# Kernel tuning notes

Measured on AMD Instinct MI355X. Metric: run time of the kernel, lower is better.

The kernel has to match this reference:

```python
import jax, jax.numpy as jnp
import numpy as np
from jax import lax

E = 8      # embed dim
H = 8      # num heads (head_dim = 1)
EPS = 1e-5


def pe_row(pos, d=E):
    # PositionalEncoding quirk: original adds pe[:, x.size(1), :] -> a SINGLE row at index L.
    i = jnp.arange(0, d, 2, dtype=jnp.float32)
    div = jnp.exp(i * (-np.log(10000.0) / d))
    row = jnp.zeros((d,), jnp.float32)
    row = row.at[0::2].set(jnp.sin(pos * div))
    row = row.at[1::2].set(jnp.cos(pos * div))
    return row


def layernorm(x, g, b):
    mu = jnp.mean(x, axis=-1, keepdims=True)
    var = jnp.mean((x - mu) ** 2, axis=-1, keepdims=True)
    return (x - mu) / jnp.sqrt(var + EPS) * g + b


def mha(q, k, v, wi, bi, wo, bo):
    # torch nn.MultiheadAttention, batch_first, eval mode (dropout off)
    d = E // H
    qp = q @ wi[:E].T + bi[:E]
    kp = k @ wi[E:2 * E].T + bi[E:2 * E]
    vp = v @ wi[2 * E:].T + bi[2 * E:]
    sh = lambda x: x.reshape(x.shape[0], x.shape[1], H, d).transpose(0, 2, 1, 3)
    qh, kh, vh = sh(qp), sh(kp), sh(vp)
    scores = jnp.einsum('bhqd,bhkd->bhqk', qh, kh) / np.sqrt(d)
    attn = jax.nn.softmax(scores, axis=-1)
    o = jnp.einsum('bhqk,bhkd->bhqd', attn, vh)
    B, _, L, _ = o.shape
    o = o.transpose(0, 2, 1, 3).reshape(B, L, E)
    return o @ wo.T + bo


def conv1d_k1p1(x, w, b):
    # Conv1d kernel_size=1, padding=1 (conv_tgt branch), then permute to (B, L, C)
    y = lax.conv_general_dilated(x, w, (1,), [(1, 1)],
                                 dimension_numbers=('NCW', 'OIW', 'NCW'))
    return (y + b[None, :, None]).transpose(0, 2, 1)


def setup_inputs() -> dict:
    key = jax.random.key(0)
    ks = jax.random.split(key, 32)
    B = 8192
    r = lambda i, shape, s=0.05: jax.random.normal(ks[i], shape, jnp.float32) * s
    return {
        'eeg': jax.random.normal(ks[0], (B, 2, 20, 118), jnp.float32),
        'pupil': jax.random.normal(ks[1], (B, 2, 30), jnp.float32),
        'speech': jax.random.normal(ks[2], (B, 2, 30), jnp.float32),
        'action': jax.random.normal(ks[3], (B, 2, 30), jnp.float32),
        'location': jax.random.normal(ks[4], (B, 3, 30), jnp.float32),
        'tgt': jax.random.normal(ks[5], (B, 30), jnp.float32),
        'eeg_conv_w': r(6, (E, 2, 20, 2), 0.1), 'eeg_conv_b': r(7, (E,)),
        'psa_conv_w': r(8, (E, 2, 1), 0.3), 'psa_conv_b': r(9, (E,)),
        'loc_conv_w': r(10, (E, 3, 1), 0.3), 'loc_conv_b': r(11, (E,)),
        'tgt_conv_w': r(12, (E, 1, 1), 0.3), 'tgt_conv_b': r(13, (E,)),
        'norm_g': jnp.ones((E,), jnp.float32), 'norm_b': jnp.zeros((E,), jnp.float32),
        'cross_in_w': r(14, (3 * E, E), 0.3), 'cross_in_b': r(15, (3 * E,)),
        'cross_out_w': r(16, (E, E), 0.3), 'cross_out_b': r(17, (E,)),
        'self_in_w': r(18, (3 * E, E), 0.3), 'self_in_b': r(19, (3 * E,)),
        'self_out_w': r(20, (E, E), 0.3), 'self_out_b': r(21, (E,)),
        'out_in_w': r(22, (3 * E, E), 0.3), 'out_in_b': r(23, (3 * E,)),
        'out_out_w': r(24, (E, E), 0.3), 'out_out_b': r(25, (E,)),
        'fc1_w': r(26, (90, 256), 0.1), 'fc1_b': r(27, (90,)),
    }


def reference(eeg, pupil, speech, action, location, tgt,
              eeg_conv_w, eeg_conv_b, psa_conv_w, psa_conv_b,
              loc_conv_w, loc_conv_b, tgt_conv_w, tgt_conv_b,
              norm_g, norm_b,
              cross_in_w, cross_in_b, cross_out_w, cross_out_b,
              self_in_w, self_in_b, self_out_w, self_out_b,
              out_in_w, out_in_b, out_out_w, out_out_b,
              fc1_w, fc1_b):
    B = eeg.shape[0]
    # eeg conv2d: (B,2,20,118) -> (B,8,1,30) -> (B,30,8)
    e = lax.conv_general_dilated(eeg, eeg_conv_w, (1, 4), 'VALID',
                                 dimension_numbers=('NCHW', 'OIHW', 'NCHW'))
    e = (e + eeg_conv_b[None, :, None, None]).squeeze(2).transpose(0, 2, 1)
    # pupil/speech/action/location (raw len 30 -> conv_tgt branch -> seq 32)
    p = conv1d_k1p1(pupil, psa_conv_w, psa_conv_b)
    s = conv1d_k1p1(speech, psa_conv_w, psa_conv_b)
    a = conv1d_k1p1(action, psa_conv_w, psa_conv_b)
    l = conv1d_k1p1(location, loc_conv_w, loc_conv_b)
    # positional encoding adds single row pe[L]
    e = e + pe_row(30.0)
    p = p + pe_row(32.0)
    s = s + pe_row(32.0)
    a = a + pe_row(32.0)
    l = l + pe_row(32.0)

    cross = lambda q, kv: mha(q, kv, kv, cross_in_w, cross_in_b, cross_out_w, cross_out_b)
    selfa = lambda x: mha(x, x, x, self_in_w, self_in_b, self_out_w, self_out_b)
    nrm = lambda x: layernorm(x, norm_g, norm_b)

    eeg_final = (nrm(cross(e, p)) + nrm(cross(e, a)) + nrm(cross(e, l))
                 + nrm(selfa(e)) + nrm(cross(e, s)))
    pupil_final = (nrm(cross(p, e)) + nrm(cross(p, a)) + nrm(cross(p, l))
                   + nrm(selfa(p)) + nrm(cross(p, s)))
    s_cross_l = nrm(cross(s, l))
    speech_final = (nrm(cross(s, e)) + nrm(cross(s, p)) + nrm(cross(s, a))
                    + s_cross_l)  # original omits speech_self
    # original bug: action_cross_location = norm(speech_cross_location)
    action_final = (nrm(cross(a, e)) + nrm(cross(a, p)) + s_cross_l
                    + nrm(selfa(a)) + nrm(cross(a, s)))
    concatenated = jnp.concatenate([eeg_final, pupil_final, action_final, speech_final], axis=1)  # (B,126,8)

    t = conv1d_k1p1(tgt[:, None, :], tgt_conv_w, tgt_conv_b)  # (B,32,8)
    t = t + pe_row(32.0)
    out = mha(t, concatenated, concatenated, out_in_w, out_in_b, out_out_w, out_out_b)  # (B,32,8)
    out = out.reshape(B, 32 * E) @ fc1_w.T + fc1_b  # (B,90)
    out = out.reshape(B, 30, 3).transpose(0, 2, 1)  # (B,3,30)
    return jax.nn.softmax(out, axis=1)
```

## Files before the change

### kernel.cpp

```cpp
#include <hip/hip_runtime.h>
#include <cstdint>
#include <cstddef>

#define NT 256
#define LOG2E 1.4426950408889634f

typedef float v2f __attribute__((ext_vector_type(2)));
typedef float v4f __attribute__((ext_vector_type(4)));

#if defined(__has_builtin)
#  if __has_builtin(__builtin_amdgcn_exp2f)
#    define EXP2F(x) __builtin_amdgcn_exp2f(x)
#  else
#    define EXP2F(x) exp2f(x)
#  endif
#else
#  define EXP2F(x) exp2f(x)
#endif

enum {
  OFF_EEGB = 0,
  OFF_PSAW = 8,
  OFF_PSAB = 24,
  OFF_LOCW = 32,
  OFF_LOCB = 56,
  OFF_TGTW = 64,
  OFF_TGTB = 72,
  OFF_NG   = 80,
  OFF_NB   = 88,
  OFF_CINW = 96,
  OFF_CINB = 288,
  OFF_COUTW= 312,
  OFF_COUTB= 376,
  OFF_SINW = 384,
  OFF_SINB = 576,
  OFF_SOUTW= 600,
  OFF_SOUTB= 664,
  OFF_OINW = 672,
  OFF_OINB = 864,
  OFF_OOUTW= 888,
  OFF_OOUTB= 952,
  OFF_FC1B = 960,
  OFF_PE30 = 1052,
  OFF_PE32 = 1060,
  OFF_Ebuf = 1068,
  OFF_Pbuf = 1308,
  OFF_Sbuf = 1564,
  OFF_Abuf = 1820,
  OFF_Lbuf = 2076,
  OFF_Tbuf = 2332,
  OFF_CAT  = 2588,
  OFF_QP   = 3596,
  OFF_KS   = 3852,
  OFF_VS   = 4396,
  OFF_FCO  = 4940,
  SM_TOTAL = 5032,
  OFF_EEGW = OFF_KS,
};

struct MhaDesc { int Lq, Lk, kstart, qoff, kvoff, wset, dst1, dst2, flags; };

#define EB 0
#define PB 30
#define AB 62
#define SB 94
static __device__ const MhaDesc g_desc[20] = {
  {30, 32, 0, OFF_Ebuf, OFF_Pbuf, 0, EB, -1, 3},
  {30, 32, 0, OFF_Ebuf, OFF_Abuf, 0, EB, -1, 3},
  {30, 32, 0, OFF_Ebuf, OFF_Lbuf, 0, EB, -1, 3},
  {30, 30, 0, OFF_Ebuf, OFF_Ebuf, 1, EB, -1, 3},
  {30, 32, 0, OFF_Ebuf, OFF_Sbuf, 0, EB, -1, 3},
  {32, 30, 0, OFF_Pbuf, OFF_Ebuf, 0, PB, -1, 3},
  {32, 32, 0, OFF_Pbuf, OFF_Abuf, 0, PB, -1, 3},
  {32, 32, 0, OFF_Pbuf, OFF_Lbuf, 0, PB, -1, 3},
  {32, 32, 0, OFF_Pbuf, OFF_Pbuf, 1, PB, -1, 3},
  {32, 32, 0, OFF_Pbuf, OFF_Sbuf, 0, PB, -1, 3},
  {32, 30, 0, OFF_Sbuf, OFF_Ebuf, 0, SB, -1, 3},
  {32, 32, 0, OFF_Sbuf, OFF_Pbuf, 0, SB, -1, 3},
  {32, 32, 0, OFF_Sbuf, OFF_Abuf, 0, SB, -1, 3},
  {32, 32, 0, OFF_Sbuf, OFF_Lbuf, 0, SB, AB, 3},
  {32, 30, 0, OFF_Abuf, OFF_Ebuf, 0, AB, -1, 3},
  {32, 32, 0, OFF_Abuf, OFF_Pbuf, 0, AB, -1, 3},
  {32, 32, 0, OFF_Abuf, OFF_Abuf, 1, AB, -1, 3},
  {32, 32, 0, OFF_Abuf, OFF_Sbuf, 0, AB, -1, 3},
  {32, 64, 0,  OFF_Tbuf, OFF_CAT, 2, -1, -1, 1},
  {32, 62, 64, OFF_Tbuf, OFF_CAT, 2, -1, -1, 2},
};

__device__ __forceinline__ float grp8_sum(float v) {
  v += __shfl_xor(v, 1);
  v += __shfl_xor(v, 2);
  v += __shfl_xor(v, 4);
  return v;
}

__device__ __forceinline__ float dot8(const float* __restrict__ x,
                                      const float* __restrict__ w, float bias) {
  v4f xa = *(const v4f*)x, xb = *(const v4f*)(x + 4);
  v4f wa = *(const v4f*)w, wb = *(const v4f*)(w + 4);
  v4f p = xa * wa;
  p += xb * wb;
  v2f q = p.xy + p.zw;
  return bias + q.x + q.y;
}

template<int LK>
__device__ __forceinline__ void attn_accum(float qq, const float* __restrict__ Kp,
                                           const float* __restrict__ Vp,
                                           v4f& l4, v4f& A4) {
  constexpr int N4 = LK >> 2;
  #pragma unroll
  for (int k4 = 0; k4 < N4; k4++) {
    v4f kk = *(const v4f*)(Kp + 4 * k4);
    v4f vv = *(const v4f*)(Vp + 4 * k4);
    v4f sc = kk * qq;
    v4f ee = { EXP2F(sc.x), EXP2F(sc.y), EXP2F(sc.z), EXP2F(sc.w) };
    l4 += ee;
    A4 += ee * vv;
  }
  if constexpr ((LK & 3) != 0) {
    v2f kk = *(const v2f*)(Kp + 4 * N4);
    v2f vv = *(const v2f*)(Vp + 4 * N4);
    v2f sc = kk * qq;
    v2f ee = { EXP2F(sc.x), EXP2F(sc.y) };
    l4.xy = l4.xy + ee;
    A4.xy = A4.xy + ee * vv;
  }
}

__global__ __launch_bounds__(NT, 8) void cmt_kernel(
    const float* __restrict__ eeg, const float* __restrict__ pupil,
    const float* __restrict__ speech, const float* __restrict__ action,
    const float* __restrict__ location, const float* __restrict__ tgt,
    const float* __restrict__ eeg_w, const float* __restrict__ eeg_b,
    const float* __restrict__ psa_w, const float* __restrict__ psa_b,
    const float* __restrict__ loc_w, const float* __restrict__ loc_b,
    const float* __restrict__ tgt_w, const float* __restrict__ tgt_b,
    const float* __restrict__ ng, const float* __restrict__ nb,
    const float* __restrict__ cin_w, const float* __restrict__ cin_b,
    const float* __restrict__ cout_w, const float* __restrict__ cout_b,
    const float* __restrict__ sin_w, const float* __restrict__ sin_b,
    const float* __restrict__ sout_w, const float* __restrict__ sout_b,
    const float* __restrict__ oin_w, const float* __restrict__ oin_b,
    const float* __restrict__ oout_w, const float* __restrict__ oout_b,
    const float* __restrict__ fc1_w, const float* __restrict__ fc1_b,
    float* __restrict__ out)
{
  __shared__ __align__(16) float sm[SM_TOTAL];
  const int tid = threadIdx.x;
  const int b = blockIdx.x;

#define CP(off, p, n) for (int i = tid; i < (n); i += NT) sm[(off)+i] = (p)[i]
#define CPQ(off, p, n, nq) for (int i = tid; i < (n); i += NT) sm[(off)+i] = (p)[i] * ((i < (nq)) ? LOG2E : 1.0f)

  for (int i = tid; i < 640; i += NT) sm[OFF_EEGW + i] = eeg_w[(i & 7) * 80 + (i >> 3)];
  CP(OFF_EEGB, eeg_b, 8);
  CP(OFF_PSAW, psa_w, 16);   CP(OFF_PSAB, psa_b, 8);
  CP(OFF_LOCW, loc_w, 24);   CP(OFF_LOCB, loc_b, 8);
  CP(OFF_TGTW, tgt_w, 8);    CP(OFF_TGTB, tgt_b, 8);
  CP(OFF_NG, ng, 8);         CP(OFF_NB, nb, 8);
  CPQ(OFF_CINW, cin_w, 192, 64);  CPQ(OFF_CINB, cin_b, 24, 8);
  CP(OFF_COUTW, cout_w, 64); CP(OFF_COUTB, cout_b, 8);
  CPQ(OFF_SINW, sin_w, 192, 64);  CPQ(OFF_SINB, sin_b, 24, 8);
  CP(OFF_SOUTW, sout_w, 64); CP(OFF_SOUTB, sout_b, 8);
  CPQ(OFF_OINW, oin_w, 192, 64);  CPQ(OFF_OINB, oin_b, 24, 8);
  CP(OFF_OOUTW, oout_w, 64); CP(OFF_OOUTB, oout_b, 8);
  CP(OFF_FC1B, fc1_b, 90);
  for (int i = tid; i < 1008; i += NT) sm[OFF_CAT + i] = 0.f;
  if (tid < 16) {
    const float divs[4] = {1.f, 0.1f, 0.01f, 0.001f};
    float pos = (tid < 8) ? 30.f : 32.f;
    int e = tid & 7;
    float x = pos * divs[e >> 1];
    float v = (e & 1) ? cosf(x) : sinf(x);
    sm[((tid < 8) ? OFF_PE30 : OFF_PE32) + e] = v;
  }
  __syncthreads();

  if (tid < 240) {
    int w = tid >> 3, o = tid & 7;
    const float* ep = eeg + (size_t)b * 4720 + 4 * w;
    const float* wt = sm + OFF_EEGW + o;
    float acc = sm[OFF_EEGB + o];
    #pragma unroll
    for (int i = 0; i < 2; i++)
      #pragma unroll
      for (int kh = 0; kh < 20; kh++) {
        float2 x = *(const float2*)(ep + i * 2360 + kh * 118);
        int ik = i * 20 + kh;
        acc = fmaf(x.x, wt[ik * 16], fmaf(x.y, wt[ik * 16 + 8], acc));
      }
    sm[OFF_Ebuf + w * 8 + o] = acc + sm[OFF_PE30 + o];
  }
  {
    int t = tid >> 3, o = tid & 7;
    bool inb = (t >= 1 && t <= 30);
    int ti = t - 1;
    float pe = sm[OFF_PE32 + o];
    float w0 = sm[OFF_PSAW + 2 * o], w1 = sm[OFF_PSAW + 2 * o + 1];
    float pb = sm[OFF_PSAB + o];
    float vp = pb, vs = pb, va = pb;
    float vl = sm[OFF_LOCB + o], vt = sm[OFF_TGTB + o];
    if (inb) {
      const float* pp = pupil    + (size_t)b * 60 + ti;
      const float* sp = speech   + (size_t)b * 60 + ti;
      const float* ap = action   + (size_t)b * 60 + ti;
      const float* lp = location + (size_t)b * 90 + ti;
      vp = fmaf(pp[0], w0, fmaf(pp[30], w1, vp));
      vs = fmaf(sp[0], w0, fmaf(sp[30], w1, vs));
      va = fmaf(ap[0], w0, fmaf(ap[30], w1, va));
      vl = fmaf(lp[0],  sm[OFF_LOCW + 3 * o],     vl);
      vl = fmaf(lp[30], sm[OFF_LOCW + 3 * o + 1], vl);
      vl = fmaf(lp[60], sm[OFF_LOCW + 3 * o + 2], vl);
      vt = fmaf(tgt[(size_t)b * 30 + ti], sm[OFF_TGTW + o], vt);
    }
    sm[OFF_Pbuf + tid] = vp + pe;
    sm[OFF_Sbuf + tid] = vs + pe;
    sm[OFF_Abuf + tid] = va + pe;
    sm[OFF_Lbuf + tid] = vl + pe;
    sm[OFF_Tbuf + tid] = vt + pe;
  }
  __syncthreads();

  float q_reg = 0.f;
  v4f l4 = {0.f, 0.f, 0.f, 0.f}, A4 = {0.f, 0.f, 0.f, 0.f};
  for (int mi = 0; mi < 20; mi++) {
    const MhaDesc d = g_desc[mi];
    int winO, binO, woutO, boutO;
    if (d.wset == 0)      { winO = OFF_CINW; binO = OFF_CINB; woutO = OFF_COUTW; boutO = OFF_COUTB; }
    else if (d.wset == 1) { winO = OFF_SINW; binO = OFF_SINB; woutO = OFF_SOUTW; boutO = OFF_SOUTB; }
    else                  { winO = OFF_OINW; binO = OFF_OINB; woutO = OFF_OOUTW; boutO = OFF_OOUTB; }

    if ((d.flags & 1) && tid < d.Lq * 8) {
      int r = tid >> 3, h = tid & 7;
      q_reg = dot8(sm + d.qoff + r * 8, sm + winO + h * 8, sm[binO + h]);
    }
    for (int idx = tid; idx < d.Lk * 8; idx += NT) {
      int r = idx >> 3, h = idx & 7;
      const float* x = sm + d.kvoff + (d.kstart + r) * 8;
      v4f xa = *(const v4f*)x, xb = *(const v4f*)(x + 4);
      const float* wk = sm + winO + 64 + h * 8;
      const float* wv = sm + winO + 128 + h * 8;
      v4f pk = xa * *(const v4f*)wk;  pk += xb * *(const v4f*)(wk + 4);
      v4f pv = xa * *(const v4f*)wv;  pv += xb * *(const v4f*)(wv + 4);
      v2f hk = pk.xy + pk.zw, hv = pv.xy + pv.zw;
      sm[OFF_KS + h * 68 + r] = sm[binO + 8 + h]  + hk.x + hk.y;
      sm[OFF_VS + h * 68 + r] = sm[binO + 16 + h] + hv.x + hv.y;
    }
    __syncthreads();

    if (tid < d.Lq * 8) {
      int e = tid & 7;
      if (d.flags & 1) { l4 = (v4f){0.f,0.f,0.f,0.f}; A4 = (v4f){0.f,0.f,0.f,0.f}; }
      const float* Kp = sm + OFF_KS + e * 68;
      const float* Vp = sm + OFF_VS + e * 68;
      switch (d.Lk) {
        case 32: attn_accum<32>(q_reg, Kp, Vp, l4, A4); break;
        case 30: attn_accum<30>(q_reg, Kp, Vp, l4, A4); break;
        case 64: attn_accum<64>(q_reg, Kp, Vp, l4, A4); break;
        case 62: attn_accum<62>(q_reg, Kp, Vp, l4, A4); break;
        default: __builtin_unreachable();
      }
      if (d.flags & 2) {
        v2f lp = l4.xy + l4.zw, ap = A4.xy + A4.zw;
        float ov = (ap.x + ap.y) * __builtin_amdgcn_rcpf(lp.x + lp.y);
        sm[OFF_QP + tid] = ov;
        int gb = tid & ~7;
        float a = dot8(sm + OFF_QP + gb, sm + woutO + e * 8, sm[boutO + e]);
        if (d.dst1 >= 0) {
          int qi = tid >> 3;
          float mu = grp8_sum(a) * 0.125f;
          float dd = a - mu;
          float var = grp8_sum(dd * dd) * 0.125f;
          float nv = fmaf(dd * rsqrtf(var + 1e-5f), sm[OFF_NG + e], sm[OFF_NB + e]);
          sm[OFF_CAT + (d.dst1 + qi) * 8 + e] += nv;
          if (d.dst2 >= 0) sm[OFF_CAT + (d.dst2 + qi) * 8 + e] += nv;
        } else {
          sm[OFF_QP + tid] = a;
        }
      }
    }
    __syncthreads();
  }

  if (tid < 180) {
    int j = tid >> 1, p = tid & 1;
    const v4f* w4 = (const v4f*)(fc1_w + j * 256);
    const v4f* o4 = (const v4f*)(sm + OFF_QP);
    v4f acc4 = {0.f, 0.f, 0.f, 0.f};
    #pragma unroll 8
    for (int c = p; c < 64; c += 2) acc4 += o4[c] * w4[c];
    v2f a2 = acc4.xy + acc4.zw;
    float acc = a2.x + a2.y;
    acc += __shfl_xor(acc, 1);
    if (p == 0) sm[OFF_FCO + j] = acc + sm[OFF_FC1B + j];
  }
  __syncthreads();
  if (tid < 30) {
    float x0 = sm[OFF_FCO + 3 * tid], x1 = sm[OFF_FCO + 3 * tid + 1], x2 = sm[OFF_FCO + 3 * tid + 2];
    float m = fmaxf(x0, fmaxf(x1, x2));
    float e0 = __expf(x0 - m), e1 = __expf(x1 - m), e2 = __expf(x2 - m);
    float inv = __builtin_amdgcn_rcpf(e0 + e1 + e2);
    float* op = out + (size_t)b * 90;
    op[tid]      = e0 * inv;
    op[30 + tid] = e1 * inv;
    op[60 + tid] = e2 * inv;
  }
#undef CP
#undef CPQ
}

extern "C" void kernel_launch(void* const* d_in, const int* in_sizes, int n_in,
                              void* d_out, int out_size, void* d_ws, size_t ws_size,
                              hipStream_t stream) {
  (void)n_in; (void)out_size; (void)d_ws; (void)ws_size;
  int B = in_sizes[0] / 4720;
  cmt_kernel<<<B, NT, 0, stream>>>(
      (const float*)d_in[0],  (const float*)d_in[1],  (const float*)d_in[2],
      (const float*)d_in[3],  (const float*)d_in[4],  (const float*)d_in[5],
      (const float*)d_in[6],  (const float*)d_in[7],  (const float*)d_in[8],
      (const float*)d_in[9],  (const float*)d_in[10], (const float*)d_in[11],
      (const float*)d_in[12], (const float*)d_in[13], (const float*)d_in[14],
      (const float*)d_in[15], (const float*)d_in[16], (const float*)d_in[17],
      (const float*)d_in[18], (const float*)d_in[19], (const float*)d_in[20],
      (const float*)d_in[21], (const float*)d_in[22], (const float*)d_in[23],
      (const float*)d_in[24], (const float*)d_in[25], (const float*)d_in[26],
      (const float*)d_in[27], (const float*)d_in[28], (const float*)d_in[29],
      (float*)d_out);
}
```

Before: 304.3 us.

## Process two queries per thread and accumulate attention outputs in registers

```diff
diff --git a/kernel.cpp b/kernel.cpp
--- a/kernel.cpp
+++ b/kernel.cpp
@@ -51,40 +51,40 @@
   OFF_Tbuf = 2332,
   OFF_CAT  = 2588,
   OFF_QP   = 3596,
-  OFF_KS   = 3852,
-  OFF_VS   = 4396,
-  OFF_FCO  = 4940,
-  SM_TOTAL = 5032,
+  OFF_KS   = 3916,
+  OFF_VS   = 4460,
+  OFF_FCO  = 5004,
+  SM_TOTAL = 5096,
   OFF_EEGW = OFF_KS,
 };
 
-struct MhaDesc { int Lq, Lk, kstart, qoff, kvoff, wset, dst1, dst2, flags; };
+struct MhaDesc { short Lq2, Lk, kstart, qoff, kvoff, wset, dst, flags; };
 
 #define EB 0
 #define PB 30
 #define AB 62
 #define SB 94
 static __device__ const MhaDesc g_desc[20] = {
-  {30, 32, 0, OFF_Ebuf, OFF_Pbuf, 0, EB, -1, 3},
-  {30, 32, 0, OFF_Ebuf, OFF_Abuf, 0, EB, -1, 3},
-  {30, 32, 0, OFF_Ebuf, OFF_Lbuf, 0, EB, -1, 3},
-  {30, 30, 0, OFF_Ebuf, OFF_Ebuf, 1, EB, -1, 3},
-  {30, 32, 0, OFF_Ebuf, OFF_Sbuf, 0, EB, -1, 3},
-  {32, 30, 0, OFF_Pbuf, OFF_Ebuf, 0, PB, -1, 3},
-  {32, 32, 0, OFF_Pbuf, OFF_Abuf, 0, PB, -1, 3},
-  {32, 32, 0, OFF_Pbuf, OFF_Lbuf, 0, PB, -1, 3},
-  {32, 32, 0, OFF_Pbuf, OFF_Pbuf, 1, PB, -1, 3},
-  {32, 32, 0, OFF_Pbuf, OFF_Sbuf, 0, PB, -1, 3},
-  {32, 30, 0, OFF_Sbuf, OFF_Ebuf, 0, SB, -1, 3},
-  {32, 32, 0, OFF_Sbuf, OFF_Pbuf, 0, SB, -1, 3},
-  {32, 32, 0, OFF_Sbuf, OFF_Abuf, 0, SB, -1, 3},
-  {32, 32, 0, OFF_Sbuf, OFF_Lbuf, 0, SB, AB, 3},
-  {32, 30, 0, OFF_Abuf, OFF_Ebuf, 0, AB, -1, 3},
-  {32, 32, 0, OFF_Abuf, OFF_Pbuf, 0, AB, -1, 3},
-  {32, 32, 0, OFF_Abuf, OFF_Abuf, 1, AB, -1, 3},
-  {32, 32, 0, OFF_Abuf, OFF_Sbuf, 0, AB, -1, 3},
-  {32, 64, 0,  OFF_Tbuf, OFF_CAT, 2, -1, -1, 1},
-  {32, 62, 64, OFF_Tbuf, OFF_CAT, 2, -1, -1, 2},
+  {15, 32, 0, OFF_Ebuf, OFF_Pbuf, 0, EB, 1|2|32},
+  {15, 32, 0, OFF_Ebuf, OFF_Abuf, 0, EB, 1|2},
+  {15, 32, 0, OFF_Ebuf, OFF_Lbuf, 0, EB, 1|2},
+  {15, 30, 0, OFF_Ebuf, OFF_Ebuf, 1, EB, 1|2},
+  {15, 32, 0, OFF_Ebuf, OFF_Sbuf, 0, EB, 1|2|4},
+  {16, 30, 0, OFF_Pbuf, OFF_Ebuf, 0, PB, 1|2|32},
+  {16, 32, 0, OFF_Pbuf, OFF_Abuf, 0, PB, 1|2},
+  {16, 32, 0, OFF_Pbuf, OFF_Lbuf, 0, PB, 1|2},
+  {16, 32, 0, OFF_Pbuf, OFF_Pbuf, 1, PB, 1|2},
+  {16, 32, 0, OFF_Pbuf, OFF_Sbuf, 0, PB, 1|2|4},
+  {16, 30, 0, OFF_Sbuf, OFF_Ebuf, 0, SB, 1|2|32},
+  {16, 32, 0, OFF_Sbuf, OFF_Pbuf, 0, SB, 1|2},
+  {16, 32, 0, OFF_Sbuf, OFF_Abuf, 0, SB, 1|2},
+  {16, 32, 0, OFF_Sbuf, OFF_Lbuf, 0, SB, 1|2|4|8},
+  {16, 30, 0, OFF_Abuf, OFF_Ebuf, 0, AB, 1|2|32},
+  {16, 32, 0, OFF_Abuf, OFF_Pbuf, 0, AB, 1|2},
+  {16, 32, 0, OFF_Abuf, OFF_Abuf, 1, AB, 1|2},
+  {16, 32, 0, OFF_Abuf, OFF_Sbuf, 0, AB, 1|2|4|16},
+  {16, 64, 0,  OFF_Tbuf, OFF_CAT, 2, -1, 1},
+  {16, 62, 64, OFF_Tbuf, OFF_CAT, 2, -1, 2},
 };
 
 __device__ __forceinline__ float grp8_sum(float v) {
@@ -97,34 +97,35 @@
 __device__ __forceinline__ float dot8(const float* __restrict__ x,
                                       const float* __restrict__ w, float bias) {
   v4f xa = *(const v4f*)x, xb = *(const v4f*)(x + 4);
-  v4f wa = *(const v4f*)w, wb = *(const v4f*)(w + 4);
-  v4f p = xa * wa;
-  p += xb * wb;
+  v4f p = xa * *(const v4f*)w;
+  p += xb * *(const v4f*)(w + 4);
   v2f q = p.xy + p.zw;
   return bias + q.x + q.y;
 }
 
 template<int LK>
-__device__ __forceinline__ void attn_accum(float qq, const float* __restrict__ Kp,
-                                           const float* __restrict__ Vp,
-                                           v4f& l4, v4f& A4) {
-  constexpr int N4 = LK >> 2;
+__device__ __forceinline__ void attn2(float q1, float q2,
+                                      const float* __restrict__ Kp,
+                                      const float* __restrict__ Vp,
+                                      v4f& la, v4f& Aa, v4f& lb, v4f& Ab) {
   #pragma unroll
-  for (int k4 = 0; k4 < N4; k4++) {
-    v4f kk = *(const v4f*)(Kp + 4 * k4);
-    v4f vv = *(const v4f*)(Vp + 4 * k4);
-    v4f sc = kk * qq;
-    v4f ee = { EXP2F(sc.x), EXP2F(sc.y), EXP2F(sc.z), EXP2F(sc.w) };
-    l4 += ee;
-    A4 += ee * vv;
+  for (int t = 0; t < (LK >> 2); t++) {
+    v4f kk = *(const v4f*)(Kp + 4 * t);
+    v4f vv = *(const v4f*)(Vp + 4 * t);
+    v4f s1 = kk * q1, s2 = kk * q2;
+    v4f e1 = { EXP2F(s1.x), EXP2F(s1.y), EXP2F(s1.z), EXP2F(s1.w) };
+    v4f e2 = { EXP2F(s2.x), EXP2F(s2.y), EXP2F(s2.z), EXP2F(s2.w) };
+    la += e1; Aa += e1 * vv;
+    lb += e2; Ab += e2 * vv;
   }
   if constexpr ((LK & 3) != 0) {
-    v2f kk = *(const v2f*)(Kp + 4 * N4);
-    v2f vv = *(const v2f*)(Vp + 4 * N4);
-    v2f sc = kk * qq;
-    v2f ee = { EXP2F(sc.x), EXP2F(sc.y) };
-    l4.xy = l4.xy + ee;
-    A4.xy = A4.xy + ee * vv;
+    v2f kk = *(const v2f*)(Kp + (LK & ~3));
+    v2f vv = *(const v2f*)(Vp + (LK & ~3));
+    v2f s1 = kk * q1, s2 = kk * q2;
+    v2f e1 = { EXP2F(s1.x), EXP2F(s1.y) };
+    v2f e2 = { EXP2F(s2.x), EXP2F(s2.y) };
+    la.xy = la.xy + e1; Aa.xy = Aa.xy + e1 * vv;
+    lb.xy = lb.xy + e2; Ab.xy = Ab.xy + e2 * vv;
   }
 }
 
@@ -153,7 +154,7 @@
 #define CP(off, p, n) for (int i = tid; i < (n); i += NT) sm[(off)+i] = (p)[i]
 #define CPQ(off, p, n, nq) for (int i = tid; i < (n); i += NT) sm[(off)+i] = (p)[i] * ((i < (nq)) ? LOG2E : 1.0f)
 
-  for (int i = tid; i < 640; i += NT) sm[OFF_EEGW + i] = eeg_w[(i & 7) * 80 + (i >> 3)];
+  for (int i = tid; i < 640; i += NT) sm[OFF_EEGW + (i / 80) * 84 + (i % 80)] = eeg_w[i];
   CP(OFF_EEGB, eeg_b, 8);
   CP(OFF_PSAW, psa_w, 16);   CP(OFF_PSAB, psa_b, 8);
   CP(OFF_LOCW, loc_w, 24);   CP(OFF_LOCB, loc_b, 8);
@@ -166,7 +167,6 @@
   CPQ(OFF_OINW, oin_w, 192, 64);  CPQ(OFF_OINB, oin_b, 24, 8);
   CP(OFF_OOUTW, oout_w, 64); CP(OFF_OOUTB, oout_b, 8);
   CP(OFF_FC1B, fc1_b, 90);
-  for (int i = tid; i < 1008; i += NT) sm[OFF_CAT + i] = 0.f;
   if (tid < 16) {
     const float divs[4] = {1.f, 0.1f, 0.01f, 0.001f};
     float pos = (tid < 8) ? 30.f : 32.f;
@@ -180,17 +180,18 @@
   if (tid < 240) {
     int w = tid >> 3, o = tid & 7;
     const float* ep = eeg + (size_t)b * 4720 + 4 * w;
-    const float* wt = sm + OFF_EEGW + o;
-    float acc = sm[OFF_EEGB + o];
+    const float* wr = sm + OFF_EEGW + o * 84;
+    v4f acc4 = {0.f, 0.f, 0.f, 0.f};
     #pragma unroll
-    for (int i = 0; i < 2; i++)
-      #pragma unroll
-      for (int kh = 0; kh < 20; kh++) {
-        float2 x = *(const float2*)(ep + i * 2360 + kh * 118);
-        int ik = i * 20 + kh;
-        acc = fmaf(x.x, wt[ik * 16], fmaf(x.y, wt[ik * 16 + 8], acc));
-      }
-    sm[OFF_Ebuf + w * 8 + o] = acc + sm[OFF_PE30 + o];
+    for (int t = 0; t < 20; t++) {
+      int ik0 = 2 * t, ik1 = 2 * t + 1;
+      float2 x0 = *(const float2*)(ep + (ik0 / 20) * 2360 + (ik0 % 20) * 118);
+      float2 x1 = *(const float2*)(ep + (ik1 / 20) * 2360 + (ik1 % 20) * 118);
+      v4f xv = {x0.x, x0.y, x1.x, x1.y};
+      acc4 += xv * *(const v4f*)(wr + 4 * t);
+    }
+    v2f s2 = acc4.xy + acc4.zw;
+    sm[OFF_Ebuf + w * 8 + o] = s2.x + s2.y + sm[OFF_EEGB + o] + sm[OFF_PE30 + o];
   }
   {
     int t = tid >> 3, o = tid & 7;
@@ -222,61 +223,96 @@
   }
   __syncthreads();
 
-  float q_reg = 0.f;
-  v4f l4 = {0.f, 0.f, 0.f, 0.f}, A4 = {0.f, 0.f, 0.f, 0.f};
+  const int qi = tid >> 3, h = tid & 7;
+  float q1 = 0.f, q2 = 0.f;
+  float cat1 = 0.f, cat2 = 0.f, car1 = 0.f, car2 = 0.f;
+  v4f la = {0.f,0.f,0.f,0.f}, Aa = la, lb = la, Ab = la;
+  float2* const qp2 = (float2*)(sm + OFF_QP);
+
   for (int mi = 0; mi < 20; mi++) {
     const MhaDesc d = g_desc[mi];
     int winO, binO, woutO, boutO;
     if (d.wset == 0)      { winO = OFF_CINW; binO = OFF_CINB; woutO = OFF_COUTW; boutO = OFF_COUTB; }
     else if (d.wset == 1) { winO = OFF_SINW; binO = OFF_SINB; woutO = OFF_SOUTW; boutO = OFF_SOUTB; }
     else                  { winO = OFF_OINW; binO = OFF_OINB; woutO = OFF_OOUTW; boutO = OFF_OOUTB; }
-
-    if ((d.flags & 1) && tid < d.Lq * 8) {
-      int r = tid >> 3, h = tid & 7;
-      q_reg = dot8(sm + d.qoff + r * 8, sm + winO + h * 8, sm[binO + h]);
-    }
-    for (int idx = tid; idx < d.Lk * 8; idx += NT) {
-      int r = idx >> 3, h = idx & 7;
-      const float* x = sm + d.kvoff + (d.kstart + r) * 8;
-      v4f xa = *(const v4f*)x, xb = *(const v4f*)(x + 4);
+    const int nact = d.Lq2 * 8;
+
+    if (d.flags & 32) { cat1 = 0.f; cat2 = 0.f; }
+
+    if ((d.flags & 1) && tid < nact) {
+      const float* w = sm + winO + h * 8;
+      float bq = sm[binO + h];
+      q1 = dot8(sm + d.qoff + qi * 8, w, bq);
+      q2 = dot8(sm + d.qoff + (qi + d.Lq2) * 8, w, bq);
+      la = (v4f){0.f,0.f,0.f,0.f}; Aa = la; lb = la; Ab = la;
+    }
+    if (tid < 128) {
       const float* wk = sm + winO + 64 + h * 8;
       const float* wv = sm + winO + 128 + h * 8;
-      v4f pk = xa * *(const v4f*)wk;  pk += xb * *(const v4f*)(wk + 4);
-      v4f pv = xa * *(const v4f*)wv;  pv += xb * *(const v4f*)(wv + 4);
-      v2f hk = pk.xy + pk.zw, hv = pv.xy + pv.zw;
-      sm[OFF_KS + h * 68 + r] = sm[binO + 8 + h]  + hk.x + hk.y;
-      sm[OFF_VS + h * 68 + r] = sm[binO + 16 + h] + hv.x + hv.y;
+      v4f ka = *(const v4f*)wk, kb = *(const v4f*)(wk + 4);
+      v4f va = *(const v4f*)wv, vb = *(const v4f*)(wv + 4);
+      float bk = sm[binO + 8 + h], bv = sm[binO + 16 + h];
+      for (int idx = tid; idx < d.Lk * 8; idx += 128) {
+        int r = idx >> 3;
+        const float* x = sm + d.kvoff + (d.kstart + r) * 8;
+        v4f xa = *(const v4f*)x, xb = *(const v4f*)(x + 4);
+        v4f pk = xa * ka; pk += xb * kb;
+        v4f pv = xa * va; pv += xb * vb;
+        v2f hk = pk.xy + pk.zw, hv = pv.xy + pv.zw;
+        sm[OFF_KS + h * 68 + r] = bk + hk.x + hk.y;
+        sm[OFF_VS + h * 68 + r] = bv + hv.x + hv.y;
+      }
     }
     __syncthreads();
 
-    if (tid < d.Lq * 8) {
-      int e = tid & 7;
-      if (d.flags & 1) { l4 = (v4f){0.f,0.f,0.f,0.f}; A4 = (v4f){0.f,0.f,0.f,0.f}; }
-      const float* Kp = sm + OFF_KS + e * 68;
-      const float* Vp = sm + OFF_VS + e * 68;
+    if (tid < nact) {
+      const float* Kp = sm + OFF_KS + h * 68;
+      const float* Vp = sm + OFF_VS + h * 68;
       switch (d.Lk) {
-        case 32: attn_accum<32>(q_reg, Kp, Vp, l4, A4); break;
-        case 30: attn_accum<30>(q_reg, Kp, Vp, l4, A4); break;
-        case 64: attn_accum<64>(q_reg, Kp, Vp, l4, A4); break;
-        case 62: attn_accum<62>(q_reg, Kp, Vp, l4, A4); break;
+        case 32: attn2<32>(q1, q2, Kp, Vp, la, Aa, lb, Ab); break;
+        case 30: attn2<30>(q1, q2, Kp, Vp, la, Aa, lb, Ab); break;
+        case 64: attn2<64>(q1, q2, Kp, Vp, la, Aa, lb, Ab); break;
+        case 62: attn2<62>(q1, q2, Kp, Vp, la, Aa, lb, Ab); break;
         default: __builtin_unreachable();
       }
       if (d.flags & 2) {
-        v2f lp = l4.xy + l4.zw, ap = A4.xy + A4.zw;
-        float ov = (ap.x + ap.y) * __builtin_amdgcn_rcpf(lp.x + lp.y);
-        sm[OFF_QP + tid] = ov;
-        int gb = tid & ~7;
-        float a = dot8(sm + OFF_QP + gb, sm + woutO + e * 8, sm[boutO + e]);
-        if (d.dst1 >= 0) {
-          int qi = tid >> 3;
-          float mu = grp8_sum(a) * 0.125f;
-          float dd = a - mu;
-          float var = grp8_sum(dd * dd) * 0.125f;
-          float nv = fmaf(dd * rsqrtf(var + 1e-5f), sm[OFF_NG + e], sm[OFF_NB + e]);
-          sm[OFF_CAT + (d.dst1 + qi) * 8 + e] += nv;
-          if (d.dst2 >= 0) sm[OFF_CAT + (d.dst2 + qi) * 8 + e] += nv;
+        v2f lp1 = la.xy + la.zw, ap1 = Aa.xy + Aa.zw;
+        v2f lp2 = lb.xy + lb.zw, ap2 = Ab.xy + Ab.zw;
+        float ov1 = (ap1.x + ap1.y) * __builtin_amdgcn_rcpf(lp1.x + lp1.y);
+        float ov2 = (ap2.x + ap2.y) * __builtin_amdgcn_rcpf(lp2.x + lp2.y);
+        qp2[qi * 10 + h] = make_float2(ov1, ov2);
+        const v4f* row = (const v4f*)(sm + OFF_QP + qi * 20);
+        v4f c0 = row[0], c1 = row[1], c2 = row[2], c3 = row[3];
+        const float* wo = sm + woutO + h * 8;
+        v4f wa = *(const v4f*)wo, wb = *(const v4f*)(wo + 4);
+        float bo = sm[boutO + h];
+        float a1 = bo, a2 = bo;
+        a1 = fmaf(c0.x, wa.x, a1); a2 = fmaf(c0.y, wa.x, a2);
+        a1 = fmaf(c0.z, wa.y, a1); a2 = fmaf(c0.w, wa.y, a2);
+        a1 = fmaf(c1.x, wa.z, a1); a2 = fmaf(c1.y, wa.z, a2);
+        a1 = fmaf(c1.z, wa.w, a1); a2 = fmaf(c1.w, wa.w, a2);
+        a1 = fmaf(c2.x, wb.x, a1); a2 = fmaf(c2.y, wb.x, a2);
+        a1 = fmaf(c2.z, wb.y, a1); a2 = fmaf(c2.w, wb.y, a2);
+        a1 = fmaf(c3.x, wb.z, a1); a2 = fmaf(c3.y, wb.z, a2);
+        a1 = fmaf(c3.z, wb.w, a1); a2 = fmaf(c3.w, wb.w, a2);
+        if (d.dst >= 0) {
+          float gg = sm[OFF_NG + h], bb = sm[OFF_NB + h];
+          float mu1 = grp8_sum(a1) * 0.125f;
+          float dd1 = a1 - mu1;
+          float nv1 = fmaf(dd1 * rsqrtf(grp8_sum(dd1 * dd1) * 0.125f + 1e-5f), gg, bb);
+          float mu2 = grp8_sum(a2) * 0.125f;
+          float dd2 = a2 - mu2;
+          float nv2 = fmaf(dd2 * rsqrtf(grp8_sum(dd2 * dd2) * 0.125f + 1e-5f), gg, bb);
+          if (d.flags & 8) { car1 = nv1; car2 = nv2; }
+          cat1 += nv1; cat2 += nv2;
+          if (d.flags & 16) { cat1 += car1; cat2 += car2; }
+          if (d.flags & 4) {
+            sm[OFF_CAT + (d.dst + qi) * 8 + h] = cat1;
+            sm[OFF_CAT + (d.dst + qi + d.Lq2) * 8 + h] = cat2;
+          }
         } else {
-          sm[OFF_QP + tid] = a;
+          sm[OFF_Tbuf + qi * 8 + h] = a1;
+          sm[OFF_Tbuf + (qi + 16) * 8 + h] = a2;
         }
       }
     }
@@ -286,7 +322,7 @@
   if (tid < 180) {
     int j = tid >> 1, p = tid & 1;
     const v4f* w4 = (const v4f*)(fc1_w + j * 256);
-    const v4f* o4 = (const v4f*)(sm + OFF_QP);
+    const v4f* o4 = (const v4f*)(sm + OFF_Tbuf);
     v4f acc4 = {0.f, 0.f, 0.f, 0.f};
     #pragma unroll 8
     for (int c = p; c < 64; c += 2) acc4 += o4[c] * w4[c];
```

Result: slower. 387.9 us (+27.5%).
